# Kernel optimization log

Measured on AMD Instinct MI355X. Metric: run time of the kernel, lower is better.

## Reference

```python
import math
import jax, jax.numpy as jnp
import numpy as np

B, S, HID = 2, 1024, 4096
NH, NKV, HD = 32, 8, 128
G = NH // NKV            # query heads per KV head (GQA group size)
PAST = 1024              # tokens already in the cache per sequence
L = PAST + S             # total KV tokens attended per sequence
SLOTS = 16384            # paged KV-cache slots (flat token addressing)
MAXPOS = 8192
THETA = 10000.0


def _rope_table():
    inv_freq = 1.0 / (THETA ** (np.arange(0, HD, 2, dtype=np.float64) / HD))
    freqs = np.arange(MAXPOS, dtype=np.float64)[:, None] * inv_freq[None, :]
    emb = np.concatenate([freqs, freqs], axis=-1)          # [MAXPOS, HD]
    return jnp.asarray(np.stack([np.cos(emb), np.sin(emb)], axis=1), jnp.float32)  # [MAXPOS,2,HD]


def setup_inputs() -> dict:
    key = jax.random.key(0)
    ks = jax.random.split(key, 6)
    hidden_states = jax.random.normal(ks[0], (B, S, HID), jnp.float32)
    kv_cache = jax.random.normal(ks[1], (SLOTS, 2, NKV, HD), jnp.float32)  # [slot, k/v, kv_head, hd]
    rope_cache = _rope_table()
    Wq = jax.random.normal(ks[2], (HID, NH * HD), jnp.float32) * 0.02
    Wk = jax.random.normal(ks[3], (HID, NKV * HD), jnp.float32) * 0.02
    Wv = jax.random.normal(ks[4], (HID, NKV * HD), jnp.float32) * 0.02
    Wo = jax.random.normal(ks[5], (NH * HD, HID), jnp.float32) * 0.02
    position_offsets = jnp.full((B,), PAST, jnp.int32)
    base = jnp.arange(B, dtype=jnp.int32)[:, None] * L            # each seq owns L contiguous slots
    kv_drain_addr_lut = base + PAST + jnp.arange(S, dtype=jnp.int32)[None, :]  # [B,S] write addrs
    kv_lut = base + jnp.arange(L, dtype=jnp.int32)[None, :]                    # [B,L] read addrs
    return {
        "hidden_states": hidden_states, "kv_cache": kv_cache, "rope_cache": rope_cache,
        "Wq": Wq, "Wk": Wk, "Wv": Wv, "Wo": Wo,
        "position_offsets": position_offsets,
        "kv_drain_addr_lut": kv_drain_addr_lut, "kv_lut": kv_lut,
    }


def _apply_rope(x, cos, sin):
    # x: [B, H, S, HD]; cos/sin: [B, 1, S, HD]
    x1, x2 = x[..., : HD // 2], x[..., HD // 2:]
    return x * cos + jnp.concatenate([-x2, x1], axis=-1) * sin


def reference(hidden_states, kv_cache, rope_cache, Wq, Wk, Wv, Wo,
              position_offsets, kv_drain_addr_lut, kv_lut):
    # QKV projections
    q = (hidden_states @ Wq).reshape(B, S, NH, HD).transpose(0, 2, 1, 3)    # [B,NH,S,HD]
    k = (hidden_states @ Wk).reshape(B, S, NKV, HD).transpose(0, 2, 1, 3)   # [B,NKV,S,HD]
    v = (hidden_states @ Wv).reshape(B, S, NKV, HD).transpose(0, 2, 1, 3)
    # RoPE at absolute positions
    pos = position_offsets[:, None] + jnp.arange(S, dtype=jnp.int32)        # [B,S]
    cos = rope_cache[pos, 0][:, None]                                       # [B,1,S,HD]
    sin = rope_cache[pos, 1][:, None]
    q = _apply_rope(q, cos, sin)
    k = _apply_rope(k, cos, sin)
    # LUT-addressed KV-cache drain (copy_kv_block)
    k_tok = k.transpose(0, 2, 1, 3).reshape(B * S, NKV, HD)
    v_tok = v.transpose(0, 2, 1, 3).reshape(B * S, NKV, HD)
    lut = kv_drain_addr_lut.reshape(-1)
    kv_cache = kv_cache.at[lut, 0].set(k_tok).at[lut, 1].set(v_tok)
    # Gather per-sequence KV pages and run grouped (GQA) causal attention
    kv = kv_cache[kv_lut]                                                   # [B,L,2,NKV,HD]
    keys = kv[:, :, 0].transpose(0, 2, 1, 3)                                # [B,NKV,L,HD]
    vals = kv[:, :, 1].transpose(0, 2, 1, 3)
    qg = q.reshape(B, NKV, G, S, HD)
    scores = jnp.einsum('bhgsd,bhld->bhgsl', qg, keys) * (HD ** -0.5)       # [B,NKV,G,S,L]
    kpos = jnp.arange(L, dtype=jnp.int32)
    causal = kpos[None, None, :] <= pos[:, :, None]                         # [B,S,L]
    scores = jnp.where(causal[:, None, None], scores, jnp.float32(-1e30))
    p = jax.nn.softmax(scores, axis=-1)
    out = jnp.einsum('bhgsl,bhld->bhgsd', p, vals).reshape(B, NH, S, HD)
    out = out.transpose(0, 2, 1, 3).reshape(B, S, HID)
    return out @ Wo
```

## Files before the change

kernel.cpp:

```cpp
#include <hip/hip_runtime.h>
#include <hip/hip_bf16.h>
#include <cstdint>
#include <cstddef>

#define B_    2
#define S_    1024
#define HID_  4096
#define NH_   32
#define NKV_  8
#define HD_   128
#define G_    4
#define PAST_ 1024
#define L_    2048
#define NQKV_ 6144

typedef __bf16 bf16_t;
typedef bf16_t bf16x4 __attribute__((ext_vector_type(4)));
typedef bf16_t bf16x8 __attribute__((ext_vector_type(8)));
typedef float  f32x4  __attribute__((ext_vector_type(4)));

__device__ __forceinline__ void gload_lds16(const bf16_t* g, bf16_t* l) {
  __builtin_amdgcn_global_load_lds(
      (const __attribute__((address_space(1))) void*)g,
      (__attribute__((address_space(3))) void*)l, 16, 0, 0);
}

__global__ __launch_bounds__(256) void cvt_bf16x8(const float* __restrict__ src,
                                                  bf16_t* __restrict__ dst) {
  size_t i = ((size_t)blockIdx.x * 256 + threadIdx.x) * 8;
  f32x4 a = *(const f32x4*)(src + i);
  f32x4 b = *(const f32x4*)(src + i + 4);
  bf16x8 o;
#pragma unroll
  for (int j = 0; j < 4; ++j) o[j] = (bf16_t)a[j];
#pragma unroll
  for (int j = 0; j < 4; ++j) o[4 + j] = (bf16_t)b[j];
  *(bf16x8*)(dst + i) = o;
}

__global__ __launch_bounds__(256) void wt_all(const float* __restrict__ Wq,
                                              const float* __restrict__ Wk,
                                              const float* __restrict__ Wv,
                                              const float* __restrict__ Wo,
                                              bf16_t* __restrict__ Wcat,
                                              bf16_t* __restrict__ Wot) {
  __shared__ float T[64][65];
  const int tid = threadIdx.x;
  const int bx = blockIdx.x;
  const float* src;
  bf16_t* dst;
  int C, c0;
  if (bx < 64)      { src = Wq; dst = Wcat;                         C = 4096; c0 = bx * 64; }
  else if (bx < 80) { src = Wk; dst = Wcat + (size_t)4096 * 4096;   C = 1024; c0 = (bx - 64) * 64; }
  else if (bx < 96) { src = Wv; dst = Wcat + (size_t)5120 * 4096;   C = 1024; c0 = (bx - 80) * 64; }
  else              { src = Wo; dst = Wot;                          C = 4096; c0 = (bx - 96) * 64; }
  const int r0 = blockIdx.y * 64;
#pragma unroll
  for (int i = 0; i < 16; ++i) {
    int idx = i * 256 + tid;
    int lr = idx >> 6, lc = idx & 63;
    T[lr][lc] = src[(size_t)(r0 + lr) * C + c0 + lc];
  }
  __syncthreads();
#pragma unroll
  for (int i = 0; i < 16; ++i) {
    int idx = i * 256 + tid;
    int lr = idx >> 6, lc = idx & 63;
    dst[(size_t)(c0 + lr) * 4096 + r0 + lc] = (bf16_t)T[lc][lr];
  }
}

template <int BN, bool OUT_BF16>
__global__ __launch_bounds__(512) void gemm8(const bf16_t* __restrict__ A,
                                             const bf16_t* __restrict__ Bt,
                                             void* __restrict__ C, int N, int K) {
  constexpr int BSLAB = BN * 32;
  constexpr int BUFE = 16384 + 2 * BSLAB;
  constexpr int NF = BN / 64;
  constexpr int WN = BN / 4;
  constexpr int BCH = BN * 4;
  __shared__ bf16_t sm[2 * BUFE];

  const int tid = threadIdx.x;
  const int lane = tid & 63;
  const int w = tid >> 6;
  const int wm = w >> 2, wn = w & 3;
  const int g = lane >> 4;
  const int r16 = lane & 15;

  const int flat = blockIdx.y * 32 + blockIdx.x;
  const int xcd = flat & 7;
  const int i2 = flat >> 3;
  const int tx = xcd * 4 + (i2 & 3);
  const int ty = i2 >> 2;
  const int m0 = ty * 256;
  const int n0 = tx * BN;

  const int NT = K >> 6;

  f32x4 acc[8][NF] = {};

  auto stageA = [&](int T, int j) {
    bf16_t* base = sm + (T & 1) * BUFE + j * 8192;
#pragma unroll
    for (int cj = 0; cj < 2; ++cj) {
      int c = (w * 2 + cj) * 64 + lane;
      int p = c * 16;
      int l = p ^ (((p >> 9) & 1) << 5);
      int row = l >> 6, colb = l & 63;
      gload_lds16(A + (size_t)(m0 + row) * K + T * 64 + j * 32 + (colb >> 1),
                  base + (w * 2 + cj) * 512);
    }
  };
  auto stageB = [&](int T, int j) {
    bf16_t* base = sm + (T & 1) * BUFE + 16384 + j * BSLAB;
#pragma unroll
    for (int cj = 0; cj < (BCH + 511) / 512; ++cj) {
      int cbase = cj * 512 + w * 64;
      if (cbase < BCH) {
        int c = cbase + lane;
        int p = c * 16;
        int l = p ^ (((p >> 9) & 1) << 5);
        int row = l >> 6, colb = l & 63;
        gload_lds16(Bt + (size_t)(n0 + row) * K + T * 64 + j * 32 + (colb >> 1),
                    base + cbase * 8);
      }
    }
  };
  auto waitbar = [&]() {
    if (BN == 192) {
      if (w < 4) asm volatile("s_waitcnt vmcnt(4)" ::: "memory");
      else       asm volatile("s_waitcnt vmcnt(3)" ::: "memory");
    } else {
      asm volatile("s_waitcnt vmcnt(3)" ::: "memory");
    }
    __builtin_amdgcn_s_barrier();
  };

  stageA(0, 0); stageB(0, 0);
  stageA(0, 1); stageB(0, 1);
  waitbar();

#pragma unroll 2
  for (int T = 0; T < NT; ++T) {
    const bf16_t* abuf = sm + (T & 1) * BUFE;
    const bf16_t* bbuf = abuf + 16384;
#pragma unroll
    for (int j = 0; j < 2; ++j) {
      const bf16_t* as = abuf + j * 8192;
      const bf16_t* bs = bbuf + j * BSLAB;
      bf16x8 af[8];
      bf16x8 bfr[NF];
#pragma unroll
      for (int m = 0; m < 8; ++m) {
        int a = (wm * 128 + m * 16 + r16) * 64 + g * 16;
        a ^= ((a >> 9) & 1) << 5;
        af[m] = *(const bf16x8*)((const char*)as + a);
      }
#pragma unroll
      for (int n = 0; n < NF; ++n) {
        int a = (wn * WN + n * 16 + r16) * 64 + g * 16;
        a ^= ((a >> 9) & 1) << 5;
        bfr[n] = *(const bf16x8*)((const char*)bs + a);
      }
      if (T + 1 < NT) { stageA(T + 1, j); stageB(T + 1, j); }
      __builtin_amdgcn_s_barrier();
      asm volatile("s_waitcnt lgkmcnt(0)" ::: "memory");
      __builtin_amdgcn_sched_barrier(0);
      __builtin_amdgcn_s_setprio(1);
#pragma unroll
      for (int m = 0; m < 8; ++m)
#pragma unroll
        for (int n = 0; n < NF; ++n)
          acc[m][n] = __builtin_amdgcn_mfma_f32_16x16x32_bf16(af[m], bfr[n],
                                                              acc[m][n], 0, 0, 0);
      __builtin_amdgcn_s_setprio(0);
      waitbar();
    }
  }

#pragma unroll
  for (int m = 0; m < 8; ++m)
#pragma unroll
    for (int n = 0; n < NF; ++n)
#pragma unroll
      for (int r = 0; r < 4; ++r) {
        int row = m0 + wm * 128 + m * 16 + g * 4 + r;
        int col = n0 + wn * WN + n * 16 + r16;
        if (OUT_BF16)
          ((bf16_t*)C)[(size_t)row * N + col] = (bf16_t)acc[m][n][r];
        else
          ((float*)C)[(size_t)row * N + col] = acc[m][n][r];
      }
}

__global__ __launch_bounds__(256) void rope_pack(const bf16_t* __restrict__ QKV,
                                                 const float* __restrict__ rope,
                                                 bf16_t* __restrict__ Qb,
                                                 bf16_t* __restrict__ Kb) {
  const int tok = blockIdx.x;
  const int head = blockIdx.y * 2 + (threadIdx.x >> 7);
  const int d = threadIdx.x & 127;
  const int b = tok >> 10, s = tok & 1023;
  const int pos = PAST_ + s;
  const int off = head < NH_ ? head * HD_ : HID_ + (head - NH_) * HD_;
  const bf16_t* row = QKV + (size_t)tok * NQKV_;
  float x = (float)row[off + d];
  int dp = d < 64 ? d + 64 : d - 64;
  float xp = (float)row[off + dp];
  float c = rope[(size_t)(pos * 2) * HD_ + d];
  float sn = rope[(size_t)(pos * 2 + 1) * HD_ + d];
  float out = d < 64 ? x * c - xp * sn : x * c + xp * sn;
  if (head < NH_)
    Qb[((size_t)(b * NH_ + head) * S_ + s) * HD_ + d] = (bf16_t)out;
  else
    Kb[((size_t)(b * NKV_ + (head - NH_)) * L_ + PAST_ + s) * HD_ + d] = (bf16_t)out;
}

__global__ __launch_bounds__(256) void past_kv(const float* __restrict__ cache,
                                               const int* __restrict__ kv_lut,
                                               bf16_t* __restrict__ Kb,
                                               bf16_t* __restrict__ Vt) {
  __shared__ bf16_t Vs[128][72];
  const int tid = threadIdx.x;
  const int lt = blockIdx.x & 15;
  const int h = (blockIdx.x >> 4) & 7;
  const int b = blockIdx.x >> 7;
  const int l0 = lt * 64;
#pragma unroll
  for (int i = 0; i < 32; ++i) {
    int idx = i * 256 + tid;
    int l = idx >> 7, d = idx & 127;
    int slot = kv_lut[b * L_ + l0 + l];
    float kv = cache[((size_t)slot * 2 * NKV_ + h) * HD_ + d];
    float vv = cache[(((size_t)slot * 2 + 1) * NKV_ + h) * HD_ + d];
    Kb[((size_t)(b * NKV_ + h) * L_ + l0 + l) * HD_ + d] = (bf16_t)kv;
    Vs[d][l] = (bf16_t)vv;
  }
  __syncthreads();
#pragma unroll
  for (int i = 0; i < 32; ++i) {
    int idx = i * 256 + tid;
    int d = idx >> 6, l = idx & 63;
    Vt[((size_t)(b * NKV_ + h) * HD_ + d) * L_ + l0 + l] = Vs[d][l];
  }
}

__global__ __launch_bounds__(256) void v_pack(const bf16_t* __restrict__ QKV,
                                              bf16_t* __restrict__ Vt) {
  __shared__ bf16_t Vs[128][72];
  const int tid = threadIdx.x;
  const int st = blockIdx.x & 15;
  const int h = (blockIdx.x >> 4) & 7;
  const int b = blockIdx.x >> 7;
  const int s0 = st * 64;
#pragma unroll
  for (int i = 0; i < 32; ++i) {
    int idx = i * 256 + tid;
    int sl = idx >> 7, d = idx & 127;
    Vs[d][sl] = QKV[(size_t)(b * S_ + s0 + sl) * NQKV_ + HID_ + NKV_ * HD_ + h * HD_ + d];
  }
  __syncthreads();
#pragma unroll
  for (int i = 0; i < 32; ++i) {
    int idx = i * 256 + tid;
    int d = idx >> 6, l = idx & 63;
    Vt[((size_t)(b * NKV_ + h) * HD_ + d) * L_ + PAST_ + s0 + l] = Vs[d][l];
  }
}

__global__ __launch_bounds__(512) void attn(const bf16_t* __restrict__ Qb,
                                            const bf16_t* __restrict__ Kb,
                                            const bf16_t* __restrict__ Vt,
                                            bf16_t* __restrict__ Ctx) {
  __shared__ bf16_t smem[40960];

  const int tid = threadIdx.x;
  const int lane = tid & 63;
  const int w = tid >> 6;
  const int g = lane >> 4;
  const int r16 = lane & 15;
  const int rx = r16 & 7;

  const int id = blockIdx.x;
  const int kh = id & 7;
  const int b = (id >> 3) & 1;
  const int qh = (id >> 4) & 3;
  const int grp = id >> 6;
  const int qc = grp < 4 ? 7 - grp : grp - 4;
  const int h = kh * G_ + qh;

  const int s0w = qc * 128 + w * 16;

  const bf16_t* qp = Qb + ((size_t)(b * NH_ + h) * S_ + s0w + r16) * HD_ + g * 8;
  bf16x8 qf[4];
#pragma unroll
  for (int ks = 0; ks < 4; ++ks) qf[ks] = *(const bf16x8*)(qp + ks * 32);

  const bf16_t* kbase = Kb + (size_t)(b * NKV_ + kh) * L_ * HD_;
  const bf16_t* vbase = Vt + (size_t)(b * NKV_ + kh) * HD_ * L_;

  const int slot0 = w * 2;
  const int kl0 = slot0 * 4 + (lane >> 4);
  const int kc0 = (lane & 15) ^ (kl0 & 7);
  const int kl1 = kl0 + 4;
  const int kc1 = (lane & 15) ^ (kl1 & 7);
  const int vd0 = slot0 * 8 + (lane >> 3);
  const int vc0 = (lane & 7) ^ (vd0 & 7);
  const int vd1 = vd0 + 8;
  const int vc1 = (lane & 7) ^ (vd1 & 7);

  float m_run = -1e30f;
  float s_run = 0.f;
  f32x4 acc_o[8] = {};

  const float scale = 0.08838834764831845f;
  const int qpos_base = PAST_ + s0w;
  const int qpos = qpos_base + r16;
  const int nt_ = 18 + 2 * qc;

  {
    bf16_t* Kd = smem;
    bf16_t* Vd = smem + 16384;
    gload_lds16(kbase + (size_t)kl0 * HD_ + kc0 * 8, Kd + slot0 * 512);
    gload_lds16(kbase + (size_t)kl1 * HD_ + kc1 * 8, Kd + (slot0 + 1) * 512);
    gload_lds16(vbase + (size_t)vd0 * L_ + vc0 * 8, Vd + slot0 * 512);
    gload_lds16(vbase + (size_t)vd1 * L_ + vc1 * 8, Vd + (slot0 + 1) * 512);
  }
  __syncthreads();

  for (int t = 0; t < nt_; ++t) {
    const int cur = t & 1;
    const int lt = t * 64;

    if (t + 1 < nt_) {
      const int ltn = lt + 64;
      bf16_t* Kd = smem + (cur ^ 1) * 8192;
      bf16_t* Vd = smem + 16384 + (cur ^ 1) * 8192;
      gload_lds16(kbase + (size_t)(ltn + kl0) * HD_ + kc0 * 8, Kd + slot0 * 512);
      gload_lds16(kbase + (size_t)(ltn + kl1) * HD_ + kc1 * 8, Kd + (slot0 + 1) * 512);
      gload_lds16(vbase + (size_t)vd0 * L_ + ltn + vc0 * 8, Vd + slot0 * 512);
      gload_lds16(vbase + (size_t)vd1 * L_ + ltn + vc1 * 8, Vd + (slot0 + 1) * 512);
    }

    const bf16_t* Kc = smem + cur * 8192;
    const bf16_t* Vc = smem + 16384 + cur * 8192;
    bf16_t* Pw = smem + 32768 + w * 1024;

    f32x4 sc[4] = {};
#pragma unroll
    for (int nt = 0; nt < 4; ++nt) {
#pragma unroll
      for (int ks = 0; ks < 4; ++ks) {
        bf16x8 kf = *(const bf16x8*)&Kc[(nt * 16 + r16) * 128 + (((ks * 4 + g) ^ rx) << 3)];
        sc[nt] = __builtin_amdgcn_mfma_f32_16x16x32_bf16(kf, qf[ks], sc[nt], 0, 0, 0);
      }
    }

    const bool need_mask = (lt + 63) > qpos_base;
    float sv[4][4];
    float tmax = -1e30f;
#pragma unroll
    for (int nt = 0; nt < 4; ++nt)
#pragma unroll
      for (int r = 0; r < 4; ++r) {
        float v = sc[nt][r] * scale;
        if (need_mask) {
          int l = lt + nt * 16 + g * 4 + r;
          if (l > qpos) v = -1e30f;
        }
        sv[nt][r] = v;
        tmax = fmaxf(tmax, v);
      }
    tmax = fmaxf(tmax, __shfl_xor(tmax, 16, 64));
    tmax = fmaxf(tmax, __shfl_xor(tmax, 32, 64));

    if (!__all(tmax <= m_run + 8.f)) {
      float newm = fmaxf(m_run, tmax);
      float alpha = __expf(m_run - newm);
      m_run = newm;
      s_run *= alpha;
#pragma unroll
      for (int r = 0; r < 4; ++r) {
        float a = __shfl(alpha, g * 4 + r, 64);
#pragma unroll
        for (int d8 = 0; d8 < 8; ++d8) acc_o[d8][r] *= a;
      }
    }

    float psum = 0.f;
#pragma unroll
    for (int nt = 0; nt < 4; ++nt) {
      bf16x4 pk;
#pragma unroll
      for (int r = 0; r < 4; ++r) {
        float pv = __expf(sv[nt][r] - m_run);
        psum += pv;
        pk[r] = (bf16_t)pv;
      }
      *(bf16x4*)&Pw[r16 * 64 + (((nt * 2 + (g >> 1)) ^ rx) << 3) + (g & 1) * 4] = pk;
    }
    psum += __shfl_xor(psum, 16, 64);
    psum += __shfl_xor(psum, 32, 64);
    s_run += psum;

#pragma unroll
    for (int ks2 = 0; ks2 < 2; ++ks2) {
      bf16x8 pa = *(const bf16x8*)&Pw[r16 * 64 + (((ks2 * 4 + g) ^ rx) << 3)];
#pragma unroll
      for (int d8 = 0; d8 < 8; ++d8) {
        bf16x8 vf = *(const bf16x8*)&Vc[(d8 * 16 + r16) * 64 + (((ks2 * 4 + g) ^ rx) << 3)];
        acc_o[d8] = __builtin_amdgcn_mfma_f32_16x16x32_bf16(pa, vf, acc_o[d8], 0, 0, 0);
      }
    }

    __syncthreads();
  }

  float inv[4];
#pragma unroll
  for (int r = 0; r < 4; ++r) inv[r] = 1.f / __shfl(s_run, g * 4 + r, 64);
#pragma unroll
  for (int d8 = 0; d8 < 8; ++d8)
#pragma unroll
    for (int r = 0; r < 4; ++r) {
      int tok = b * S_ + s0w + g * 4 + r;
      int col = h * HD_ + d8 * 16 + r16;
      Ctx[(size_t)tok * HID_ + col] = (bf16_t)(acc_o[d8][r] * inv[r]);
    }
}

extern "C" void kernel_launch(void* const* d_in, const int* in_sizes, int n_in,
                              void* d_out, int out_size, void* d_ws, size_t ws_size,
                              hipStream_t stream) {
  const float* hidden = (const float*)d_in[0];
  const float* kv_cache = (const float*)d_in[1];
  const float* rope = (const float*)d_in[2];
  const float* Wq = (const float*)d_in[3];
  const float* Wk = (const float*)d_in[4];
  const float* Wv = (const float*)d_in[5];
  const float* Wo = (const float*)d_in[6];
  const int* kv_lut = (const int*)d_in[9];
  float* out = (float*)d_out;

  bf16_t* Xb = (bf16_t*)d_ws;
  bf16_t* Wcat = Xb + (size_t)2048 * 4096;
  bf16_t* Wot = Wcat + (size_t)6144 * 4096;
  bf16_t* QKVb = Wot + (size_t)4096 * 4096;
  bf16_t* Qb = QKVb + (size_t)2048 * 6144;
  bf16_t* Kb = Qb + (size_t)B_ * NH_ * S_ * HD_;
  bf16_t* Vt = Kb + (size_t)B_ * NKV_ * L_ * HD_;
  bf16_t* Ctx = Xb;

  cvt_bf16x8<<<4096, 256, 0, stream>>>(hidden, Xb);
  wt_all<<<dim3(160, 64), 256, 0, stream>>>(Wq, Wk, Wv, Wo, Wcat, Wot);

  gemm8<192, true><<<dim3(32, 8), 512, 0, stream>>>(Xb, Wcat, QKVb, NQKV_, HID_);

  rope_pack<<<dim3(2048, 20), 256, 0, stream>>>(QKVb, rope, Qb, Kb);
  past_kv<<<256, 256, 0, stream>>>(kv_cache, kv_lut, Kb, Vt);
  v_pack<<<256, 256, 0, stream>>>(QKVb, Vt);

  attn<<<512, 512, 0, stream>>>(Qb, Kb, Vt, Ctx);

  gemm8<128, false><<<dim3(32, 8), 512, 0, stream>>>(Ctx, Wot, out, HID_, HID_);
}
```

Baseline: 350.1 us.

## Vectorize weight transpose, trim GEMM barriers, and shuffle P in registers for attention

The weight transpose/convert kernel now uses float4 loads and 4-wide bf16 stores instead of scalar accesses. The GEMM inner loop drops the extra barrier, lgkmcnt wait and sched_barrier before the MFMAs, leaving only the barrier in waitbar. In attention, the probability tile is redistributed between lanes with cross-lane shuffles instead of going through LDS. This cuts shared memory use, and the launch bounds now request more resident blocks. Removing the GEMM synchronisation risks reading LDS before other waves' fragment reads complete, and the shuffles add ALU work.

```diff
diff --git a/kernel.cpp b/kernel.cpp
--- a/kernel.cpp
+++ b/kernel.cpp
@@ -18,6 +18,7 @@
 typedef bf16_t bf16x4 __attribute__((ext_vector_type(4)));
 typedef bf16_t bf16x8 __attribute__((ext_vector_type(8)));
 typedef float  f32x4  __attribute__((ext_vector_type(4)));
+typedef unsigned short ushort4_t __attribute__((ext_vector_type(4)));
 
 __device__ __forceinline__ void gload_lds16(const bf16_t* g, bf16_t* l) {
   __builtin_amdgcn_global_load_lds(
@@ -55,18 +56,27 @@
   else if (bx < 96) { src = Wv; dst = Wcat + (size_t)5120 * 4096;   C = 1024; c0 = (bx - 80) * 64; }
   else              { src = Wo; dst = Wot;                          C = 4096; c0 = (bx - 96) * 64; }
   const int r0 = blockIdx.y * 64;
-#pragma unroll
-  for (int i = 0; i < 16; ++i) {
-    int idx = i * 256 + tid;
-    int lr = idx >> 6, lc = idx & 63;
-    T[lr][lc] = src[(size_t)(r0 + lr) * C + c0 + lc];
+  const int rr = tid >> 4;
+  const int c4 = tid & 15;
+#pragma unroll
+  for (int i = 0; i < 4; ++i) {
+    int row = i * 16 + rr;
+    f32x4 v = *(const f32x4*)&src[(size_t)(r0 + row) * C + c0 + c4 * 4];
+#pragma unroll
+    for (int e = 0; e < 4; ++e) T[row][c4 * 4 + e] = v[e];
   }
   __syncthreads();
 #pragma unroll
-  for (int i = 0; i < 16; ++i) {
-    int idx = i * 256 + tid;
-    int lr = idx >> 6, lc = idx & 63;
-    dst[(size_t)(c0 + lr) * 4096 + r0 + lc] = (bf16_t)T[lc][lr];
+  for (int i = 0; i < 4; ++i) {
+    int orow = i * 16 + rr;
+    ushort4_t o;
+#pragma unroll
+    for (int e = 0; e < 4; ++e) {
+      union { bf16_t b; unsigned short u; } cv;
+      cv.b = (bf16_t)T[c4 * 4 + e][orow];
+      o[e] = cv.u;
+    }
+    *(ushort4_t*)&dst[(size_t)(c0 + orow) * 4096 + r0 + c4 * 4] = o;
   }
 }
 
@@ -134,7 +144,7 @@
     } else {
       asm volatile("s_waitcnt vmcnt(3)" ::: "memory");
     }
-    __builtin_amdgcn_s_barrier();
+    asm volatile("s_barrier" ::: "memory");
   };
 
   stageA(0, 0); stageB(0, 0);
@@ -164,9 +174,6 @@
         bfr[n] = *(const bf16x8*)((const char*)bs + a);
       }
       if (T + 1 < NT) { stageA(T + 1, j); stageB(T + 1, j); }
-      __builtin_amdgcn_s_barrier();
-      asm volatile("s_waitcnt lgkmcnt(0)" ::: "memory");
-      __builtin_amdgcn_sched_barrier(0);
       __builtin_amdgcn_s_setprio(1);
 #pragma unroll
       for (int m = 0; m < 8; ++m)
@@ -269,11 +276,11 @@
   }
 }
 
-__global__ __launch_bounds__(512) void attn(const bf16_t* __restrict__ Qb,
-                                            const bf16_t* __restrict__ Kb,
-                                            const bf16_t* __restrict__ Vt,
-                                            bf16_t* __restrict__ Ctx) {
-  __shared__ bf16_t smem[40960];
+__global__ __launch_bounds__(512, 4) void attn(const bf16_t* __restrict__ Qb,
+                                               const bf16_t* __restrict__ Kb,
+                                               const bf16_t* __restrict__ Vt,
+                                               bf16_t* __restrict__ Ctx) {
+  __shared__ bf16_t smem[32768];
 
   const int tid = threadIdx.x;
   const int lane = tid & 63;
@@ -345,7 +352,6 @@
 
     const bf16_t* Kc = smem + cur * 8192;
     const bf16_t* Vc = smem + 16384 + cur * 8192;
-    bf16_t* Pw = smem + 32768 + w * 1024;
 
     f32x4 sc[4] = {};
 #pragma unroll
@@ -388,29 +394,45 @@
       }
     }
 
+    uint32_t pkw[4][2];
     float psum = 0.f;
 #pragma unroll
     for (int nt = 0; nt < 4; ++nt) {
-      bf16x4 pk;
+      union { bf16_t bh[4]; uint32_t u[2]; } pk;
 #pragma unroll
       for (int r = 0; r < 4; ++r) {
         float pv = __expf(sv[nt][r] - m_run);
         psum += pv;
-        pk[r] = (bf16_t)pv;
-      }
-      *(bf16x4*)&Pw[r16 * 64 + (((nt * 2 + (g >> 1)) ^ rx) << 3) + (g & 1) * 4] = pk;
+        pk.bh[r] = (bf16_t)pv;
+      }
+      pkw[nt][0] = pk.u[0];
+      pkw[nt][1] = pk.u[1];
     }
     psum += __shfl_xor(psum, 16, 64);
     psum += __shfl_xor(psum, 32, 64);
     s_run += psum;
 
+    const bool hi = (g & 2) != 0;
+    const int srcA = ((g & 1) << 5) + r16;
 #pragma unroll
     for (int ks2 = 0; ks2 < 2; ++ks2) {
-      bf16x8 pa = *(const bf16x8*)&Pw[r16 * 64 + (((ks2 * 4 + g) ^ rx) << 3)];
+      uint32_t a00 = (uint32_t)__shfl((int)pkw[2 * ks2][0],     srcA,      64);
+      uint32_t a01 = (uint32_t)__shfl((int)pkw[2 * ks2][1],     srcA,      64);
+      uint32_t b00 = (uint32_t)__shfl((int)pkw[2 * ks2 + 1][0], srcA,      64);
+      uint32_t b01 = (uint32_t)__shfl((int)pkw[2 * ks2 + 1][1], srcA,      64);
+      uint32_t a10 = (uint32_t)__shfl((int)pkw[2 * ks2][0],     srcA + 16, 64);
+      uint32_t a11 = (uint32_t)__shfl((int)pkw[2 * ks2][1],     srcA + 16, 64);
+      uint32_t b10 = (uint32_t)__shfl((int)pkw[2 * ks2 + 1][0], srcA + 16, 64);
+      uint32_t b11 = (uint32_t)__shfl((int)pkw[2 * ks2 + 1][1], srcA + 16, 64);
+      union { uint32_t u[4]; bf16x8 v; } pa;
+      pa.u[0] = hi ? b00 : a00;
+      pa.u[1] = hi ? b01 : a01;
+      pa.u[2] = hi ? b10 : a10;
+      pa.u[3] = hi ? b11 : a11;
 #pragma unroll
       for (int d8 = 0; d8 < 8; ++d8) {
         bf16x8 vf = *(const bf16x8*)&Vc[(d8 * 16 + r16) * 64 + (((ks2 * 4 + g) ^ rx) << 3)];
-        acc_o[d8] = __builtin_amdgcn_mfma_f32_16x16x32_bf16(pa, vf, acc_o[d8], 0, 0, 0);
+        acc_o[d8] = __builtin_amdgcn_mfma_f32_16x16x32_bf16(pa.v, vf, acc_o[d8], 0, 0, 0);
       }
     }
 
```

Measured after the change: 354.7 us. Within noise of the previous version (+1.3%).
